# Kernel optimization log

Hardware: AMD Instinct MI355X
Metric: run time of the kernel (lower is better)

The kernel has to match this reference:

```python
import jax, jax.numpy as jnp
import numpy as np


def _dfb_filter():
    v = np.array([0.63, -0.193, 0.0972, -0.0526, 0.0272, -0.0144], dtype=np.float32)
    f = np.concatenate((v[::-1], v))
    f[::2] = -f[::2]
    return jnp.asarray(f)


def _resampm(x, type_, shift=1):
    # periodic shear along rows: out[..., i, j] = x[..., (i + k_j) % m, j]
    m, n = x.shape[-2], x.shape[-1]
    j = jnp.arange(n)
    k = (shift * j) % m if type_ == 1 else (-shift * j) % m
    rows = (jnp.arange(m)[:, None] + k[None, :]) % m  # [m, n]
    return x[..., rows, j[None, :]]


def _resamp(x, type_, shift=1):
    if type_ in (1, 2):
        return _resampm(x, type_, shift)
    return _resampm(x.swapaxes(-2, -1), type_ - 2, shift).swapaxes(-2, -1)


def _slice_1r(y):
    # interleave rows: [0, m, 1, m+1, ...]
    m = y.shape[-2] // 2
    a, b = y[..., :m, :], y[..., m:, :]
    return jnp.stack([a, b], axis=-2).reshape(y.shape)


def _slice_2c(y):
    # interleave cols: [0, n, 1, n+1, ...]
    n = y.shape[-1] // 2
    a, b = y[..., :n], y[..., n:]
    return jnp.stack([a, b], axis=-1).reshape(y.shape)


def _extend2(x, ru, rd, cl, cr, extmod):
    rx, cx = x.shape[-2], x.shape[-1]
    if extmod == 'per':
        y = jnp.concatenate([x[..., rx - ru:, :], x, x[..., :rd, :]], axis=-2)
    elif extmod == 'qper_col':
        cx2 = cx // 2  # cx is even here
        xs = jnp.concatenate([x[..., cx2:], x[..., :cx2]], axis=-1)
        y = jnp.concatenate([xs[..., rx - ru:, :], x, xs[..., :rd, :]], axis=-2)
    else:
        raise ValueError(extmod)
    return jnp.concatenate([y[..., cx - cl:], y, y[..., :cr]], axis=-1)


def _sep_conv(y, f):
    # depthwise separable filtering (torch used a dense diagonal kernel -> identical math)
    L = f.shape[0]
    ch = y.shape[1]
    dn = ('NCHW', 'OIHW', 'NCHW')
    kh = jnp.broadcast_to(f.reshape(1, 1, L, 1), (ch, 1, L, 1))
    y = jax.lax.conv_general_dilated(y, kh, (1, 1), 'VALID', dimension_numbers=dn, feature_group_count=ch)
    kw = jnp.broadcast_to(f.reshape(1, 1, 1, L), (ch, 1, 1, L))
    return jax.lax.conv_general_dilated(y, kw, (1, 1), 'VALID', dimension_numbers=dn, feature_group_count=ch)


def _sefilter2(x, f, extmod='per', shift=(0, 0)):
    L = f.shape[0]
    lf = (L - 1) / 2  # 5.5 for the 12-tap filter
    ru = int(np.floor(lf)) + shift[0]
    rd = int(np.ceil(lf)) - shift[0]
    cl = int(np.floor(lf)) + shift[1]
    cr = int(np.ceil(lf)) - shift[1]
    y = _extend2(x, ru, rd, cl, cr, extmod)
    return _sep_conv(y, f)


def _qprec(p0, p1, type2):
    if type2 == '1r':
        a = _resamp(p0, 4)
        b = jnp.roll(_resamp(p1, 4), 1, axis=-1)
        y = _slice_1r(jnp.concatenate([a, b], axis=-2))
        return _resamp(y, 1)
    elif type2 == '2c':
        a = _resamp(p0, 2)
        b = jnp.roll(_resamp(p1, 2), 1, axis=-2)
        y = _slice_2c(jnp.concatenate([a, b], axis=-1))
        return _resamp(y, 3)
    raise ValueError(type2)


def _fbrec(y0, y1, f, type2, extmod):
    p1 = -(2.0 ** -0.5) * (y1 + _sefilter2(y0, f, extmod))
    p0 = (2.0 ** 0.5) * y0 + _sefilter2(p1, f, extmod, (1, 1))
    return _qprec(p0, p1, type2)


def _dfbrec4(y0, y1, y2, y3):
    # dfbrec_layer for n=2 (4 directional subbands):
    # list reorder y[2:] = y[-1:1:-1] -> [y0, y1, y3, y2]; rebacksamp is a no-op for n=2.
    f = _dfb_filter()
    C = y0.shape[1]
    # new_fbrec_layer([y[1], y[3]], [y[0], y[2]], f, 'q', '2c', 'per')  (channel-batched)
    Y0 = jnp.concatenate([y1, y2], axis=1)
    Y1 = jnp.concatenate([y0, y3], axis=1)
    x = _fbrec(Y0, Y1, f, '2c', 'per')  # [N, 2C, H, 2W]
    x0, x1 = x[:, :C], x[:, C:]
    # fbrec_layer(x0, x1, f, 'q', '1r', 'qper_col')  -> [N, C, 2H, 2W]
    return _fbrec(x0, x1, f, '1r', 'qper_col')


def setup_inputs() -> dict:
    key = jax.random.key(0)
    ks = jax.random.split(key, 4)
    shp = (8, 32, 128, 128)
    return {('y%d' % i): jax.random.normal(ks[i], shp, dtype=jnp.float32) for i in range(4)}


def reference(y0, y1, y2, y3):
    return _dfbrec4(y0, y1, y2, y3)
```

## Files before the change

### kernel.cpp

```cpp
#include <hip/hip_runtime.h>

namespace {

constexpr float FF[12] = {0.0144f, 0.0272f, 0.0526f, 0.0972f, 0.193f, 0.63f,
                          -0.63f, -0.193f, -0.0972f, -0.0526f, -0.0272f, -0.0144f};
constexpr float SQ2   = 1.41421356237309515f;
constexpr float NISQ2 = -0.70710678118654752f;

template <int O, int W4>
__device__ __forceinline__ float4 hconv(const float4* R4, int row4, int j4) {
  float r[20];
#pragma unroll
  for (int d = 0; d < 5; ++d) {
    float4 t = R4[row4 + ((j4 + d - 2) & (W4 - 1))];
    r[4 * d + 0] = t.x; r[4 * d + 1] = t.y; r[4 * d + 2] = t.z; r[4 * d + 3] = t.w;
  }
  float4 o = make_float4(0.f, 0.f, 0.f, 0.f);
#pragma unroll
  for (int a = 0; a < 12; ++a) {
    const float fa = FF[a];
    o.x += fa * r[8 + 0 + a - O];
    o.y += fa * r[8 + 1 + a - O];
    o.z += fa * r[8 + 2 + a - O];
    o.w += fa * r[8 + 3 + a - O];
  }
  return o;
}

template <int O>
__device__ __forceinline__ float4 vconv_s1(const float4* S4, int i, int j4) {
  float4 o = make_float4(0.f, 0.f, 0.f, 0.f);
#pragma unroll
  for (int a = 0; a < 12; ++a) {
    const float fa = FF[a];
    float4 v = S4[((i + a - O) & 127) * 32 + j4];
    o.x += fa * v.x; o.y += fa * v.y; o.z += fa * v.z; o.w += fa * v.w;
  }
  return o;
}

template <int O>
__device__ __forceinline__ float4 vconv_s2(const float4* S4, int i, int j4) {
  float4 o = make_float4(0.f, 0.f, 0.f, 0.f);
#pragma unroll
  for (int a = 0; a < 12; ++a) {
    const float fa = FF[a];
    int r = i + a - O;
    int idx = ((unsigned)r < 128u) ? (r * 64 + j4) : ((r & 127) * 64 + (j4 ^ 32));
    float4 v = S4[idx];
    o.x += fa * v.x; o.y += fa * v.y; o.z += fa * v.z; o.w += fa * v.w;
  }
  return o;
}

}

__global__ __launch_bounds__(1024) void s1_kernel(
    const float* __restrict__ y0, const float* __restrict__ y1,
    const float* __restrict__ y2, const float* __restrict__ y3,
    float* __restrict__ xout) {
  __shared__ float bufA[16384];
  __shared__ float bufB[16384];
  float4* A4 = reinterpret_cast<float4*>(bufA);
  float4* B4 = reinterpret_cast<float4*>(bufB);

  const int p  = blockIdx.x;
  const int b  = p >> 6;
  const int cc = p & 63;
  const int sub = (b * 32 + (cc & 31)) << 14;
  const float* Y0 = (cc < 32 ? y1 : y2) + sub;
  const float* Y1 = (cc < 32 ? y0 : y3) + sub;
  const float4* Y04 = reinterpret_cast<const float4*>(Y0);
  const float4* Y14 = reinterpret_cast<const float4*>(Y1);
  float* xp = xout + (size_t)p * 32768;

  const int tid = threadIdx.x;

#pragma unroll
  for (int k = 0; k < 4; ++k) A4[tid + k * 1024] = Y04[tid + k * 1024];
  __syncthreads();

#pragma unroll
  for (int k = 0; k < 4; ++k) {
    int g = tid + k * 1024;
    B4[g] = vconv_s1<5>(A4, g >> 5, g & 31);
  }
  __syncthreads();

#pragma unroll
  for (int k = 0; k < 4; ++k) {
    int g = tid + k * 1024;
    int i = g >> 5, j4 = g & 31;
    float4 h = hconv<5, 32>(B4, i * 32, j4);
    float4 yv = Y14[g];
    float4 o;
    o.x = NISQ2 * (yv.x + h.x);
    o.y = NISQ2 * (yv.y + h.y);
    o.z = NISQ2 * (yv.z + h.z);
    o.w = NISQ2 * (yv.w + h.w);
    A4[g] = o;
  }
  __syncthreads();

#pragma unroll
  for (int k = 0; k < 4; ++k) {
    int g = tid + k * 1024;
    B4[g] = vconv_s1<6>(A4, g >> 5, g & 31);
  }
  __syncthreads();

  float4 pv[4];
#pragma unroll
  for (int k = 0; k < 4; ++k) {
    int g = tid + k * 1024;
    int i = g >> 5, j4 = g & 31;
    float4 h = hconv<6, 32>(B4, i * 32, j4);
    float4 yv = Y04[g];
    pv[k].x = SQ2 * yv.x + h.x;
    pv[k].y = SQ2 * yv.y + h.y;
    pv[k].z = SQ2 * yv.z + h.z;
    pv[k].w = SQ2 * yv.w + h.w;
  }
  __syncthreads();
#pragma unroll
  for (int k = 0; k < 4; ++k) B4[tid + k * 1024] = pv[k];
  __syncthreads();

#pragma unroll
  for (int k = 0; k < 8; ++k) {
    int t = tid + k * 1024;
    int i = t >> 6;
    int j4b = (t & 63) << 2;
    float tmp[4];
#pragma unroll
    for (int m = 0; m < 4; ++m) {
      int jo = j4b + m;
      int J = (i + jo) & 255;
      int c = J >> 1;
      float v;
      if (J & 1) {
        int r = (i - 1 - c) & 127;
        v = bufA[r * 128 + c];
      } else {
        int r = (i - c) & 127;
        v = bufB[r * 128 + c];
      }
      tmp[m] = v;
    }
    reinterpret_cast<float4*>(xp)[t] = make_float4(tmp[0], tmp[1], tmp[2], tmp[3]);
  }
}

__global__ __launch_bounds__(1024) void s2_kernel(const float* __restrict__ x,
                                                  float* __restrict__ out) {
  __shared__ float buf[32768];
  float4* X4 = reinterpret_cast<float4*>(buf);

  const int q = blockIdx.x;
  const int b = q >> 5, c = q & 31;
  const float* x0 = x + (size_t)(b * 64 + c) * 32768;
  const float* x1 = x + (size_t)(b * 64 + 32 + c) * 32768;
  const float4* x04 = reinterpret_cast<const float4*>(x0);
  const float4* x14 = reinterpret_cast<const float4*>(x1);
  float* op = out + (size_t)q * 65536;

  const int tid = threadIdx.x;
  float4 tv[8];

#pragma unroll
  for (int k = 0; k < 8; ++k) X4[tid + k * 1024] = x04[tid + k * 1024];
  __syncthreads();

#pragma unroll
  for (int k = 0; k < 8; ++k) {
    int g = tid + k * 1024;
    tv[k] = vconv_s2<5>(X4, g >> 6, g & 63);
  }
  __syncthreads();
#pragma unroll
  for (int k = 0; k < 8; ++k) X4[tid + k * 1024] = tv[k];
  __syncthreads();

#pragma unroll
  for (int k = 0; k < 8; ++k) {
    int g = tid + k * 1024;
    int i = g >> 6, j4 = g & 63;
    float4 h = hconv<5, 64>(X4, i * 64, j4);
    float4 xv = x14[g];
    tv[k].x = NISQ2 * (xv.x + h.x);
    tv[k].y = NISQ2 * (xv.y + h.y);
    tv[k].z = NISQ2 * (xv.z + h.z);
    tv[k].w = NISQ2 * (xv.w + h.w);
  }
  __syncthreads();
#pragma unroll
  for (int k = 0; k < 8; ++k) X4[tid + k * 1024] = tv[k];
  __syncthreads();

#pragma unroll
  for (int k = 0; k < 32; ++k) {
    int t = tid + k * 1024;
    int i = t >> 7;
    int u = t & 127;
    int jo = (u << 1) | ((i + 1) & 1);
    int r = ((i + jo) & 255) >> 1;
    int cc2 = (jo - 1 - r) & 255;
    op[i * 256 + jo] = buf[r * 256 + cc2];
  }

#pragma unroll
  for (int k = 0; k < 8; ++k) {
    int g = tid + k * 1024;
    tv[k] = vconv_s2<6>(X4, g >> 6, g & 63);
  }
  __syncthreads();
#pragma unroll
  for (int k = 0; k < 8; ++k) X4[tid + k * 1024] = tv[k];
  __syncthreads();

#pragma unroll
  for (int k = 0; k < 8; ++k) {
    int g = tid + k * 1024;
    int i = g >> 6, j4 = g & 63;
    float4 h = hconv<6, 64>(X4, i * 64, j4);
    float4 xv = x04[g];
    tv[k].x = SQ2 * xv.x + h.x;
    tv[k].y = SQ2 * xv.y + h.y;
    tv[k].z = SQ2 * xv.z + h.z;
    tv[k].w = SQ2 * xv.w + h.w;
  }
  __syncthreads();
#pragma unroll
  for (int k = 0; k < 8; ++k) X4[tid + k * 1024] = tv[k];
  __syncthreads();

#pragma unroll
  for (int k = 0; k < 32; ++k) {
    int t = tid + k * 1024;
    int i = t >> 7;
    int u = t & 127;
    int jo = (u << 1) | (i & 1);
    int r = ((i + jo) & 255) >> 1;
    int cc2 = (jo - r) & 255;
    op[i * 256 + jo] = buf[r * 256 + cc2];
  }
}

extern "C" void kernel_launch(void* const* d_in, const int* in_sizes, int n_in,
                              void* d_out, int out_size, void* d_ws, size_t ws_size,
                              hipStream_t stream) {
  const float* y0 = (const float*)d_in[0];
  const float* y1 = (const float*)d_in[1];
  const float* y2 = (const float*)d_in[2];
  const float* y3 = (const float*)d_in[3];
  float* xws = (float*)d_ws;
  float* outp = (float*)d_out;

  s1_kernel<<<512, 1024, 0, stream>>>(y0, y1, y2, y3, xws);
  s2_kernel<<<256, 1024, 0, stream>>>(xws, outp);
}
```

Baseline: 196.3 us.

## Register-block separable convolutions, pad shared rows, single buffer, vectorized output stores

Both kernels now compute the vertical filter with each thread producing 8 consecutive rows from a 19-row sliding window, and the horizontal filter with each thread producing 32 consecutive outputs from a 48-float register window. The aim is to cut redundant shared-memory reads. Shared rows are padded (stride 33/65 float4) to avoid bank conflicts, and s1 drops to one buffer with 512 threads. The odd-phase output values are gathered into registers before the buffer is overwritten, so the final write can emit interleaved float4 stores instead of scalar or split writes. The cost is higher register pressure (48-float windows plus 32 saved values), which may limit occupancy despite the launch-bounds hints.

```diff
diff --git a/kernel.cpp b/kernel.cpp
--- a/kernel.cpp
+++ b/kernel.cpp
@@ -7,62 +7,19 @@
 constexpr float SQ2   = 1.41421356237309515f;
 constexpr float NISQ2 = -0.70710678118654752f;
 
-template <int O, int W4>
-__device__ __forceinline__ float4 hconv(const float4* R4, int row4, int j4) {
-  float r[20];
-#pragma unroll
-  for (int d = 0; d < 5; ++d) {
-    float4 t = R4[row4 + ((j4 + d - 2) & (W4 - 1))];
-    r[4 * d + 0] = t.x; r[4 * d + 1] = t.y; r[4 * d + 2] = t.z; r[4 * d + 3] = t.w;
-  }
-  float4 o = make_float4(0.f, 0.f, 0.f, 0.f);
-#pragma unroll
-  for (int a = 0; a < 12; ++a) {
-    const float fa = FF[a];
-    o.x += fa * r[8 + 0 + a - O];
-    o.y += fa * r[8 + 1 + a - O];
-    o.z += fa * r[8 + 2 + a - O];
-    o.w += fa * r[8 + 3 + a - O];
-  }
-  return o;
-}
-
-template <int O>
-__device__ __forceinline__ float4 vconv_s1(const float4* S4, int i, int j4) {
-  float4 o = make_float4(0.f, 0.f, 0.f, 0.f);
-#pragma unroll
-  for (int a = 0; a < 12; ++a) {
-    const float fa = FF[a];
-    float4 v = S4[((i + a - O) & 127) * 32 + j4];
-    o.x += fa * v.x; o.y += fa * v.y; o.z += fa * v.z; o.w += fa * v.w;
-  }
-  return o;
-}
-
-template <int O>
-__device__ __forceinline__ float4 vconv_s2(const float4* S4, int i, int j4) {
-  float4 o = make_float4(0.f, 0.f, 0.f, 0.f);
-#pragma unroll
-  for (int a = 0; a < 12; ++a) {
-    const float fa = FF[a];
-    int r = i + a - O;
-    int idx = ((unsigned)r < 128u) ? (r * 64 + j4) : ((r & 127) * 64 + (j4 ^ 32));
-    float4 v = S4[idx];
-    o.x += fa * v.x; o.y += fa * v.y; o.z += fa * v.z; o.w += fa * v.w;
-  }
-  return o;
-}
-
-}
-
-__global__ __launch_bounds__(1024) void s1_kernel(
+__device__ __forceinline__ void fma4(float4& o, float s, const float4& v) {
+  o.x += s * v.x; o.y += s * v.y; o.z += s * v.z; o.w += s * v.w;
+}
+
+}
+
+__global__ __launch_bounds__(512, 4) void s1_kernel(
     const float* __restrict__ y0, const float* __restrict__ y1,
     const float* __restrict__ y2, const float* __restrict__ y3,
     float* __restrict__ xout) {
-  __shared__ float bufA[16384];
-  __shared__ float bufB[16384];
-  float4* A4 = reinterpret_cast<float4*>(bufA);
-  float4* B4 = reinterpret_cast<float4*>(bufB);
+  __shared__ float bufF[128 * 132];
+  float4* buf4 = reinterpret_cast<float4*>(bufF);
+  constexpr int SG = 33;
 
   const int p  = blockIdx.x;
   const int b  = p >> 6;
@@ -72,177 +29,341 @@
   const float* Y1 = (cc < 32 ? y0 : y3) + sub;
   const float4* Y04 = reinterpret_cast<const float4*>(Y0);
   const float4* Y14 = reinterpret_cast<const float4*>(Y1);
-  float* xp = xout + (size_t)p * 32768;
+  float4* xp4 = reinterpret_cast<float4*>(xout + (size_t)p * 32768);
 
   const int tid = threadIdx.x;
 
 #pragma unroll
-  for (int k = 0; k < 4; ++k) A4[tid + k * 1024] = Y04[tid + k * 1024];
-  __syncthreads();
-
-#pragma unroll
-  for (int k = 0; k < 4; ++k) {
-    int g = tid + k * 1024;
-    B4[g] = vconv_s1<5>(A4, g >> 5, g & 31);
-  }
-  __syncthreads();
-
-#pragma unroll
-  for (int k = 0; k < 4; ++k) {
-    int g = tid + k * 1024;
-    int i = g >> 5, j4 = g & 31;
-    float4 h = hconv<5, 32>(B4, i * 32, j4);
-    float4 yv = Y14[g];
-    float4 o;
-    o.x = NISQ2 * (yv.x + h.x);
-    o.y = NISQ2 * (yv.y + h.y);
-    o.z = NISQ2 * (yv.z + h.z);
-    o.w = NISQ2 * (yv.w + h.w);
-    A4[g] = o;
-  }
-  __syncthreads();
-
-#pragma unroll
-  for (int k = 0; k < 4; ++k) {
-    int g = tid + k * 1024;
-    B4[g] = vconv_s1<6>(A4, g >> 5, g & 31);
-  }
-  __syncthreads();
-
-  float4 pv[4];
-#pragma unroll
-  for (int k = 0; k < 4; ++k) {
-    int g = tid + k * 1024;
-    int i = g >> 5, j4 = g & 31;
-    float4 h = hconv<6, 32>(B4, i * 32, j4);
-    float4 yv = Y04[g];
-    pv[k].x = SQ2 * yv.x + h.x;
-    pv[k].y = SQ2 * yv.y + h.y;
-    pv[k].z = SQ2 * yv.z + h.z;
-    pv[k].w = SQ2 * yv.w + h.w;
-  }
-  __syncthreads();
-#pragma unroll
-  for (int k = 0; k < 4; ++k) B4[tid + k * 1024] = pv[k];
-  __syncthreads();
-
-#pragma unroll
   for (int k = 0; k < 8; ++k) {
-    int t = tid + k * 1024;
-    int i = t >> 6;
-    int j4b = (t & 63) << 2;
-    float tmp[4];
-#pragma unroll
-    for (int m = 0; m < 4; ++m) {
-      int jo = j4b + m;
-      int J = (i + jo) & 255;
+    int idx = tid + k * 512;
+    buf4[(idx >> 5) * SG + (idx & 31)] = Y04[idx];
+  }
+  __syncthreads();
+
+  {
+    const int j4 = tid & 31;
+    const int i0 = (tid >> 5) * 8;
+    float4 acc[8];
+#pragma unroll
+    for (int k = 0; k < 8; ++k) acc[k] = make_float4(0.f, 0.f, 0.f, 0.f);
+#pragma unroll
+    for (int d = 0; d < 19; ++d) {
+      int r = (i0 - 5 + d) & 127;
+      float4 v = buf4[r * SG + j4];
+#pragma unroll
+      for (int k = 0; k < 8; ++k) {
+        int a = d - k;
+        if (a >= 0 && a < 12) fma4(acc[k], FF[a], v);
+      }
+    }
+    __syncthreads();
+#pragma unroll
+    for (int k = 0; k < 8; ++k) buf4[(i0 + k) * SG + j4] = acc[k];
+  }
+  __syncthreads();
+
+  {
+    const int i  = tid >> 2;
+    const int g0 = (tid & 3) * 8;
+    float w[48];
+#pragma unroll
+    for (int d = 0; d < 12; ++d) {
+      float4 v = buf4[i * SG + ((g0 - 2 + d) & 31)];
+      w[4 * d + 0] = v.x; w[4 * d + 1] = v.y; w[4 * d + 2] = v.z; w[4 * d + 3] = v.w;
+    }
+    float4 pv[8];
+#pragma unroll
+    for (int mg = 0; mg < 8; ++mg) {
+      float4 yv = Y14[i * 32 + g0 + mg];
+      float o0 = 0.f, o1 = 0.f, o2 = 0.f, o3 = 0.f;
+#pragma unroll
+      for (int a = 0; a < 12; ++a) {
+        const float fa = FF[a];
+        o0 += fa * w[3 + 4 * mg + 0 + a];
+        o1 += fa * w[3 + 4 * mg + 1 + a];
+        o2 += fa * w[3 + 4 * mg + 2 + a];
+        o3 += fa * w[3 + 4 * mg + 3 + a];
+      }
+      pv[mg].x = NISQ2 * (yv.x + o0);
+      pv[mg].y = NISQ2 * (yv.y + o1);
+      pv[mg].z = NISQ2 * (yv.z + o2);
+      pv[mg].w = NISQ2 * (yv.w + o3);
+    }
+    __syncthreads();
+#pragma unroll
+    for (int mg = 0; mg < 8; ++mg) buf4[i * SG + g0 + mg] = pv[mg];
+  }
+  __syncthreads();
+
+  float xodd[32];
+  {
+#pragma unroll
+    for (int k = 0; k < 16; ++k) {
+      int t = tid + k * 512;
+      int i2 = t >> 6;
+      int j4o = t & 63;
+      int m0 = 1 - (i2 & 1);
+#pragma unroll
+      for (int h = 0; h < 2; ++h) {
+        int jo = 4 * j4o + m0 + 2 * h;
+        int J = (i2 + jo) & 255;
+        int c = J >> 1;
+        int r = (i2 - 1 - c) & 127;
+        xodd[2 * k + h] = bufF[r * 132 + c];
+      }
+    }
+    const int j4 = tid & 31;
+    const int i0 = (tid >> 5) * 8;
+    float4 acc[8];
+#pragma unroll
+    for (int k = 0; k < 8; ++k) acc[k] = make_float4(0.f, 0.f, 0.f, 0.f);
+#pragma unroll
+    for (int d = 0; d < 19; ++d) {
+      int r = (i0 - 6 + d) & 127;
+      float4 v = buf4[r * SG + j4];
+#pragma unroll
+      for (int k = 0; k < 8; ++k) {
+        int a = d - k;
+        if (a >= 0 && a < 12) fma4(acc[k], FF[a], v);
+      }
+    }
+    __syncthreads();
+#pragma unroll
+    for (int k = 0; k < 8; ++k) buf4[(i0 + k) * SG + j4] = acc[k];
+  }
+  __syncthreads();
+
+  {
+    const int i  = tid >> 2;
+    const int g0 = (tid & 3) * 8;
+    float w[48];
+#pragma unroll
+    for (int d = 0; d < 12; ++d) {
+      float4 v = buf4[i * SG + ((g0 - 2 + d) & 31)];
+      w[4 * d + 0] = v.x; w[4 * d + 1] = v.y; w[4 * d + 2] = v.z; w[4 * d + 3] = v.w;
+    }
+    float4 pv[8];
+#pragma unroll
+    for (int mg = 0; mg < 8; ++mg) {
+      float4 yv = Y04[i * 32 + g0 + mg];
+      float o0 = 0.f, o1 = 0.f, o2 = 0.f, o3 = 0.f;
+#pragma unroll
+      for (int a = 0; a < 12; ++a) {
+        const float fa = FF[a];
+        o0 += fa * w[2 + 4 * mg + 0 + a];
+        o1 += fa * w[2 + 4 * mg + 1 + a];
+        o2 += fa * w[2 + 4 * mg + 2 + a];
+        o3 += fa * w[2 + 4 * mg + 3 + a];
+      }
+      pv[mg].x = SQ2 * yv.x + o0;
+      pv[mg].y = SQ2 * yv.y + o1;
+      pv[mg].z = SQ2 * yv.z + o2;
+      pv[mg].w = SQ2 * yv.w + o3;
+    }
+    __syncthreads();
+#pragma unroll
+    for (int mg = 0; mg < 8; ++mg) buf4[i * SG + g0 + mg] = pv[mg];
+  }
+  __syncthreads();
+
+#pragma unroll
+  for (int k = 0; k < 16; ++k) {
+    int t = tid + k * 512;
+    int i2 = t >> 6;
+    int j4o = t & 63;
+    float ev[2];
+#pragma unroll
+    for (int h = 0; h < 2; ++h) {
+      int me = (i2 & 1) + 2 * h;
+      int jo = 4 * j4o + me;
+      int J = (i2 + jo) & 255;
       int c = J >> 1;
-      float v;
-      if (J & 1) {
-        int r = (i - 1 - c) & 127;
-        v = bufA[r * 128 + c];
-      } else {
-        int r = (i - c) & 127;
-        v = bufB[r * 128 + c];
-      }
-      tmp[m] = v;
-    }
-    reinterpret_cast<float4*>(xp)[t] = make_float4(tmp[0], tmp[1], tmp[2], tmp[3]);
-  }
-}
-
-__global__ __launch_bounds__(1024) void s2_kernel(const float* __restrict__ x,
-                                                  float* __restrict__ out) {
-  __shared__ float buf[32768];
-  float4* X4 = reinterpret_cast<float4*>(buf);
+      int r = (i2 - c) & 127;
+      ev[h] = bufF[r * 132 + c];
+    }
+    float o0 = xodd[2 * k + 0], o1 = xodd[2 * k + 1];
+    bool sw = (i2 & 1) != 0;
+    float t0 = sw ? o0 : ev[0];
+    float t1 = sw ? ev[0] : o0;
+    float t2 = sw ? o1 : ev[1];
+    float t3 = sw ? ev[1] : o1;
+    xp4[t] = make_float4(t0, t1, t2, t3);
+  }
+}
+
+__global__ __launch_bounds__(1024, 4) void s2_kernel(const float* __restrict__ x,
+                                                     float* __restrict__ out) {
+  __shared__ float bufF[128 * 260];
+  float4* buf4 = reinterpret_cast<float4*>(bufF);
+  constexpr int SG = 65;
 
   const int q = blockIdx.x;
   const int b = q >> 5, c = q & 31;
-  const float* x0 = x + (size_t)(b * 64 + c) * 32768;
-  const float* x1 = x + (size_t)(b * 64 + 32 + c) * 32768;
-  const float4* x04 = reinterpret_cast<const float4*>(x0);
-  const float4* x14 = reinterpret_cast<const float4*>(x1);
-  float* op = out + (size_t)q * 65536;
+  const float4* x04 = reinterpret_cast<const float4*>(x + (size_t)(b * 64 + c) * 32768);
+  const float4* x14 = reinterpret_cast<const float4*>(x + (size_t)(b * 64 + 32 + c) * 32768);
+  float4* op4 = reinterpret_cast<float4*>(out + (size_t)q * 65536);
 
   const int tid = threadIdx.x;
-  float4 tv[8];
-
-#pragma unroll
-  for (int k = 0; k < 8; ++k) X4[tid + k * 1024] = x04[tid + k * 1024];
-  __syncthreads();
 
 #pragma unroll
   for (int k = 0; k < 8; ++k) {
-    int g = tid + k * 1024;
-    tv[k] = vconv_s2<5>(X4, g >> 6, g & 63);
-  }
-  __syncthreads();
-#pragma unroll
-  for (int k = 0; k < 8; ++k) X4[tid + k * 1024] = tv[k];
-  __syncthreads();
-
-#pragma unroll
-  for (int k = 0; k < 8; ++k) {
-    int g = tid + k * 1024;
-    int i = g >> 6, j4 = g & 63;
-    float4 h = hconv<5, 64>(X4, i * 64, j4);
-    float4 xv = x14[g];
-    tv[k].x = NISQ2 * (xv.x + h.x);
-    tv[k].y = NISQ2 * (xv.y + h.y);
-    tv[k].z = NISQ2 * (xv.z + h.z);
-    tv[k].w = NISQ2 * (xv.w + h.w);
-  }
-  __syncthreads();
-#pragma unroll
-  for (int k = 0; k < 8; ++k) X4[tid + k * 1024] = tv[k];
-  __syncthreads();
-
-#pragma unroll
-  for (int k = 0; k < 32; ++k) {
+    int idx = tid + k * 1024;
+    buf4[(idx >> 6) * SG + (idx & 63)] = x04[idx];
+  }
+  __syncthreads();
+
+  {
+    const int j4 = tid & 63;
+    const int i0 = (tid >> 6) * 8;
+    float4 acc[8];
+#pragma unroll
+    for (int k = 0; k < 8; ++k) acc[k] = make_float4(0.f, 0.f, 0.f, 0.f);
+#pragma unroll
+    for (int d = 0; d < 19; ++d) {
+      int rr = i0 - 5 + d;
+      int r = rr & 127;
+      int g = ((unsigned)rr < 128u) ? j4 : (j4 ^ 32);
+      float4 v = buf4[r * SG + g];
+#pragma unroll
+      for (int k = 0; k < 8; ++k) {
+        int a = d - k;
+        if (a >= 0 && a < 12) fma4(acc[k], FF[a], v);
+      }
+    }
+    __syncthreads();
+#pragma unroll
+    for (int k = 0; k < 8; ++k) buf4[(i0 + k) * SG + j4] = acc[k];
+  }
+  __syncthreads();
+
+  {
+    const int i  = tid >> 3;
+    const int g0 = (tid & 7) * 8;
+    float w[48];
+#pragma unroll
+    for (int d = 0; d < 12; ++d) {
+      float4 v = buf4[i * SG + ((g0 - 2 + d) & 63)];
+      w[4 * d + 0] = v.x; w[4 * d + 1] = v.y; w[4 * d + 2] = v.z; w[4 * d + 3] = v.w;
+    }
+    float4 pv[8];
+#pragma unroll
+    for (int mg = 0; mg < 8; ++mg) {
+      float4 xv = x14[i * 64 + g0 + mg];
+      float o0 = 0.f, o1 = 0.f, o2 = 0.f, o3 = 0.f;
+#pragma unroll
+      for (int a = 0; a < 12; ++a) {
+        const float fa = FF[a];
+        o0 += fa * w[3 + 4 * mg + 0 + a];
+        o1 += fa * w[3 + 4 * mg + 1 + a];
+        o2 += fa * w[3 + 4 * mg + 2 + a];
+        o3 += fa * w[3 + 4 * mg + 3 + a];
+      }
+      pv[mg].x = NISQ2 * (xv.x + o0);
+      pv[mg].y = NISQ2 * (xv.y + o1);
+      pv[mg].z = NISQ2 * (xv.z + o2);
+      pv[mg].w = NISQ2 * (xv.w + o3);
+    }
+    __syncthreads();
+#pragma unroll
+    for (int mg = 0; mg < 8; ++mg) buf4[i * SG + g0 + mg] = pv[mg];
+  }
+  __syncthreads();
+
+  float oodd[32];
+  {
+#pragma unroll
+    for (int k = 0; k < 16; ++k) {
+      int t = tid + k * 1024;
+      int i2 = t >> 6;
+      int j4o = t & 63;
+      int m0 = 1 - (i2 & 1);
+#pragma unroll
+      for (int h = 0; h < 2; ++h) {
+        int jo = 4 * j4o + m0 + 2 * h;
+        int I = (i2 + jo) & 255;
+        int r2 = I >> 1;
+        int c2 = (jo - 1 - r2) & 255;
+        oodd[2 * k + h] = bufF[r2 * 260 + c2];
+      }
+    }
+    const int j4 = tid & 63;
+    const int i0 = (tid >> 6) * 8;
+    float4 acc[8];
+#pragma unroll
+    for (int k = 0; k < 8; ++k) acc[k] = make_float4(0.f, 0.f, 0.f, 0.f);
+#pragma unroll
+    for (int d = 0; d < 19; ++d) {
+      int rr = i0 - 6 + d;
+      int r = rr & 127;
+      int g = ((unsigned)rr < 128u) ? j4 : (j4 ^ 32);
+      float4 v = buf4[r * SG + g];
+#pragma unroll
+      for (int k = 0; k < 8; ++k) {
+        int a = d - k;
+        if (a >= 0 && a < 12) fma4(acc[k], FF[a], v);
+      }
+    }
+    __syncthreads();
+#pragma unroll
+    for (int k = 0; k < 8; ++k) buf4[(i0 + k) * SG + j4] = acc[k];
+  }
+  __syncthreads();
+
+  {
+    const int i  = tid >> 3;
+    const int g0 = (tid & 7) * 8;
+    float w[48];
+#pragma unroll
+    for (int d = 0; d < 12; ++d) {
+      float4 v = buf4[i * SG + ((g0 - 2 + d) & 63)];
+      w[4 * d + 0] = v.x; w[4 * d + 1] = v.y; w[4 * d + 2] = v.z; w[4 * d + 3] = v.w;
+    }
+    float4 pv[8];
+#pragma unroll
+    for (int mg = 0; mg < 8; ++mg) {
+      float4 xv = x04[i * 64 + g0 + mg];
+      float o0 = 0.f, o1 = 0.f, o2 = 0.f, o3 = 0.f;
+#pragma unroll
+      for (int a = 0; a < 12; ++a) {
+        const float fa = FF[a];
+        o0 += fa * w[2 + 4 * mg + 0 + a];
+        o1 += fa * w[2 + 4 * mg + 1 + a];
+        o2 += fa * w[2 + 4 * mg + 2 + a];
+        o3 += fa * w[2 + 4 * mg + 3 + a];
+      }
+      pv[mg].x = SQ2 * xv.x + o0;
+      pv[mg].y = SQ2 * xv.y + o1;
+      pv[mg].z = SQ2 * xv.z + o2;
+      pv[mg].w = SQ2 * xv.w + o3;
+    }
+    __syncthreads();
+#pragma unroll
+    for (int mg = 0; mg < 8; ++mg) buf4[i * SG + g0 + mg] = pv[mg];
+  }
+  __syncthreads();
+
+#pragma unroll
+  for (int k = 0; k < 16; ++k) {
     int t = tid + k * 1024;
-    int i = t >> 7;
-    int u = t & 127;
-    int jo = (u << 1) | ((i + 1) & 1);
-    int r = ((i + jo) & 255) >> 1;
-    int cc2 = (jo - 1 - r) & 255;
-    op[i * 256 + jo] = buf[r * 256 + cc2];
-  }
-
-#pragma unroll
-  for (int k = 0; k < 8; ++k) {
-    int g = tid + k * 1024;
-    tv[k] = vconv_s2<6>(X4, g >> 6, g & 63);
-  }
-  __syncthreads();
-#pragma unroll
-  for (int k = 0; k < 8; ++k) X4[tid + k * 1024] = tv[k];
-  __syncthreads();
-
-#pragma unroll
-  for (int k = 0; k < 8; ++k) {
-    int g = tid + k * 1024;
-    int i = g >> 6, j4 = g & 63;
-    float4 h = hconv<6, 64>(X4, i * 64, j4);
-    float4 xv = x04[g];
-    tv[k].x = SQ2 * xv.x + h.x;
-    tv[k].y = SQ2 * xv.y + h.y;
-    tv[k].z = SQ2 * xv.z + h.z;
-    tv[k].w = SQ2 * xv.w + h.w;
-  }
-  __syncthreads();
-#pragma unroll
-  for (int k = 0; k < 8; ++k) X4[tid + k * 1024] = tv[k];
-  __syncthreads();
-
-#pragma unroll
-  for (int k = 0; k < 32; ++k) {
-    int t = tid + k * 1024;
-    int i = t >> 7;
-    int u = t & 127;
-    int jo = (u << 1) | (i & 1);
-    int r = ((i + jo) & 255) >> 1;
-    int cc2 = (jo - r) & 255;
-    op[i * 256 + jo] = buf[r * 256 + cc2];
+    int i2 = t >> 6;
+    int j4o = t & 63;
+    float ev[2];
+#pragma unroll
+    for (int h = 0; h < 2; ++h) {
+      int me = (i2 & 1) + 2 * h;
+      int jo = 4 * j4o + me;
+      int I = (i2 + jo) & 255;
+      int r2 = I >> 1;
+      int c2 = (jo - r2) & 255;
+      ev[h] = bufF[r2 * 260 + c2];
+    }
+    float o0 = oodd[2 * k + 0], o1 = oodd[2 * k + 1];
+    bool sw = (i2 & 1) != 0;
+    float t0 = sw ? o0 : ev[0];
+    float t1 = sw ? ev[0] : o0;
+    float t2 = sw ? o1 : ev[1];
+    float t3 = sw ? ev[1] : o1;
+    op4[t] = make_float4(t0, t1, t2, t3);
   }
 }
 
@@ -256,6 +377,6 @@
   float* xws = (float*)d_ws;
   float* outp = (float*)d_out;
 
-  s1_kernel<<<512, 1024, 0, stream>>>(y0, y1, y2, y3, xws);
+  s1_kernel<<<512, 512, 0, stream>>>(y0, y1, y2, y3, xws);
   s2_kernel<<<256, 1024, 0, stream>>>(xws, outp);
 }
```

Measured after the change: 201.4 us. +2.6%, slower.

## Fuse separable convolutions into register-blocked row sweeps with padded single LDS buffer

Applied to the files above, without the earlier changes.

Restructures both kernels so each thread computes an 8-row strip. It applies the horizontal filter per input row and accumulates the vertical filter in registers across a 19-row sliding window. This removes the intermediate LDS round trips and barriers between the vertical and horizontal passes, and the first pass now reads straight from global memory. A single padded LDS buffer replaces the two buffers to cut bank conflicts, and output stores become float4 writes that interleave odd and even phases held in registers. The price is some redundant horizontal work per strip, higher register pressure from the accumulators and saved odd values, and a smaller s1 block size.

```diff
diff --git a/kernel.cpp b/kernel.cpp
--- a/kernel.cpp
+++ b/kernel.cpp
@@ -7,242 +7,261 @@
 constexpr float SQ2   = 1.41421356237309515f;
 constexpr float NISQ2 = -0.70710678118654752f;
 
-template <int O, int W4>
-__device__ __forceinline__ float4 hconv(const float4* R4, int row4, int j4) {
-  float r[20];
-#pragma unroll
-  for (int d = 0; d < 5; ++d) {
-    float4 t = R4[row4 + ((j4 + d - 2) & (W4 - 1))];
-    r[4 * d + 0] = t.x; r[4 * d + 1] = t.y; r[4 * d + 2] = t.z; r[4 * d + 3] = t.w;
-  }
+__device__ __forceinline__ void fma4(float4& o, float s, const float4& v) {
+  o.x += s * v.x; o.y += s * v.y; o.z += s * v.z; o.w += s * v.w;
+}
+
+template <int SH>
+__device__ __forceinline__ float4 hrow_conv(const float* w) {
   float4 o = make_float4(0.f, 0.f, 0.f, 0.f);
 #pragma unroll
   for (int a = 0; a < 12; ++a) {
     const float fa = FF[a];
-    o.x += fa * r[8 + 0 + a - O];
-    o.y += fa * r[8 + 1 + a - O];
-    o.z += fa * r[8 + 2 + a - O];
-    o.w += fa * r[8 + 3 + a - O];
+    o.x += fa * w[SH + 0 + a];
+    o.y += fa * w[SH + 1 + a];
+    o.z += fa * w[SH + 2 + a];
+    o.w += fa * w[SH + 3 + a];
   }
   return o;
 }
 
-template <int O>
-__device__ __forceinline__ float4 vconv_s1(const float4* S4, int i, int j4) {
-  float4 o = make_float4(0.f, 0.f, 0.f, 0.f);
-#pragma unroll
-  for (int a = 0; a < 12; ++a) {
-    const float fa = FF[a];
-    float4 v = S4[((i + a - O) & 127) * 32 + j4];
-    o.x += fa * v.x; o.y += fa * v.y; o.z += fa * v.z; o.w += fa * v.w;
-  }
-  return o;
-}
-
-template <int O>
-__device__ __forceinline__ float4 vconv_s2(const float4* S4, int i, int j4) {
-  float4 o = make_float4(0.f, 0.f, 0.f, 0.f);
-#pragma unroll
-  for (int a = 0; a < 12; ++a) {
-    const float fa = FF[a];
-    int r = i + a - O;
-    int idx = ((unsigned)r < 128u) ? (r * 64 + j4) : ((r & 127) * 64 + (j4 ^ 32));
-    float4 v = S4[idx];
-    o.x += fa * v.x; o.y += fa * v.y; o.z += fa * v.z; o.w += fa * v.w;
-  }
-  return o;
-}
-
-}
-
-__global__ __launch_bounds__(1024) void s1_kernel(
+}
+
+__global__ __launch_bounds__(512, 4) void s1_kernel(
     const float* __restrict__ y0, const float* __restrict__ y1,
     const float* __restrict__ y2, const float* __restrict__ y3,
     float* __restrict__ xout) {
-  __shared__ float bufA[16384];
-  __shared__ float bufB[16384];
-  float4* A4 = reinterpret_cast<float4*>(bufA);
-  float4* B4 = reinterpret_cast<float4*>(bufB);
+  __shared__ float bufF[128 * 132];
+  float4* buf4 = reinterpret_cast<float4*>(bufF);
+  constexpr int SG = 33;
 
   const int p  = blockIdx.x;
   const int b  = p >> 6;
   const int cc = p & 63;
   const int sub = (b * 32 + (cc & 31)) << 14;
-  const float* Y0 = (cc < 32 ? y1 : y2) + sub;
-  const float* Y1 = (cc < 32 ? y0 : y3) + sub;
-  const float4* Y04 = reinterpret_cast<const float4*>(Y0);
-  const float4* Y14 = reinterpret_cast<const float4*>(Y1);
-  float* xp = xout + (size_t)p * 32768;
+  const float4* Y04 = reinterpret_cast<const float4*>((cc < 32 ? y1 : y2) + sub);
+  const float4* Y14 = reinterpret_cast<const float4*>((cc < 32 ? y0 : y3) + sub);
+  float4* xp4 = reinterpret_cast<float4*>(xout + (size_t)p * 32768);
 
   const int tid = threadIdx.x;
-
-#pragma unroll
-  for (int k = 0; k < 4; ++k) A4[tid + k * 1024] = Y04[tid + k * 1024];
-  __syncthreads();
-
-#pragma unroll
-  for (int k = 0; k < 4; ++k) {
-    int g = tid + k * 1024;
-    B4[g] = vconv_s1<5>(A4, g >> 5, g & 31);
-  }
-  __syncthreads();
-
-#pragma unroll
-  for (int k = 0; k < 4; ++k) {
-    int g = tid + k * 1024;
-    int i = g >> 5, j4 = g & 31;
-    float4 h = hconv<5, 32>(B4, i * 32, j4);
-    float4 yv = Y14[g];
-    float4 o;
-    o.x = NISQ2 * (yv.x + h.x);
-    o.y = NISQ2 * (yv.y + h.y);
-    o.z = NISQ2 * (yv.z + h.z);
-    o.w = NISQ2 * (yv.w + h.w);
-    A4[g] = o;
-  }
-  __syncthreads();
-
-#pragma unroll
-  for (int k = 0; k < 4; ++k) {
-    int g = tid + k * 1024;
-    B4[g] = vconv_s1<6>(A4, g >> 5, g & 31);
-  }
-  __syncthreads();
-
-  float4 pv[4];
-#pragma unroll
-  for (int k = 0; k < 4; ++k) {
-    int g = tid + k * 1024;
-    int i = g >> 5, j4 = g & 31;
-    float4 h = hconv<6, 32>(B4, i * 32, j4);
-    float4 yv = Y04[g];
-    pv[k].x = SQ2 * yv.x + h.x;
-    pv[k].y = SQ2 * yv.y + h.y;
-    pv[k].z = SQ2 * yv.z + h.z;
-    pv[k].w = SQ2 * yv.w + h.w;
-  }
-  __syncthreads();
-#pragma unroll
-  for (int k = 0; k < 4; ++k) B4[tid + k * 1024] = pv[k];
-  __syncthreads();
-
-#pragma unroll
-  for (int k = 0; k < 8; ++k) {
-    int t = tid + k * 1024;
-    int i = t >> 6;
-    int j4b = (t & 63) << 2;
-    float tmp[4];
-#pragma unroll
-    for (int m = 0; m < 4; ++m) {
-      int jo = j4b + m;
-      int J = (i + jo) & 255;
-      int c = J >> 1;
-      float v;
-      if (J & 1) {
-        int r = (i - 1 - c) & 127;
-        v = bufA[r * 128 + c];
-      } else {
-        int r = (i - c) & 127;
-        v = bufB[r * 128 + c];
-      }
-      tmp[m] = v;
-    }
-    reinterpret_cast<float4*>(xp)[t] = make_float4(tmp[0], tmp[1], tmp[2], tmp[3]);
-  }
-}
-
-__global__ __launch_bounds__(1024) void s2_kernel(const float* __restrict__ x,
-                                                  float* __restrict__ out) {
-  __shared__ float buf[32768];
-  float4* X4 = reinterpret_cast<float4*>(buf);
+  const int j  = tid & 31;
+  const int i0 = (tid >> 5) * 8;
+
+  float4 acc[8];
+#pragma unroll
+  for (int k = 0; k < 8; ++k) acc[k] = make_float4(0.f, 0.f, 0.f, 0.f);
+#pragma unroll
+  for (int d = 0; d < 19; ++d) {
+    const int r = (i0 + d - 5) & 127;
+    float w[20];
+#pragma unroll
+    for (int dg = 0; dg < 5; ++dg) {
+      float4 v = Y04[r * 32 + ((j + dg - 2) & 31)];
+      w[4 * dg + 0] = v.x; w[4 * dg + 1] = v.y; w[4 * dg + 2] = v.z; w[4 * dg + 3] = v.w;
+    }
+    const float4 h = hrow_conv<3>(w);
+#pragma unroll
+    for (int k = 0; k < 8; ++k) {
+      const int a = d - k;
+      if (a >= 0 && a < 12) fma4(acc[k], FF[a], h);
+    }
+  }
+#pragma unroll
+  for (int k = 0; k < 8; ++k) {
+    float4 yv = Y14[(i0 + k) * 32 + j];
+    float4 pv;
+    pv.x = NISQ2 * (yv.x + acc[k].x);
+    pv.y = NISQ2 * (yv.y + acc[k].y);
+    pv.z = NISQ2 * (yv.z + acc[k].z);
+    pv.w = NISQ2 * (yv.w + acc[k].w);
+    buf4[(i0 + k) * SG + j] = pv;
+  }
+  __syncthreads();
+
+  float xodd[32];
+#pragma unroll
+  for (int k = 0; k < 16; ++k) {
+    const int t = tid + k * 512;
+    const int i2 = t >> 6, j4o = t & 63;
+    const int m0 = 1 - (i2 & 1);
+#pragma unroll
+    for (int h = 0; h < 2; ++h) {
+      const int jo = 4 * j4o + m0 + 2 * h;
+      const int J = (i2 + jo) & 255;
+      const int c = J >> 1;
+      const int r = (i2 - 1 - c) & 127;
+      xodd[2 * k + h] = bufF[r * 132 + c];
+    }
+  }
+#pragma unroll
+  for (int k = 0; k < 8; ++k) acc[k] = make_float4(0.f, 0.f, 0.f, 0.f);
+#pragma unroll
+  for (int d = 0; d < 19; ++d) {
+    const int r = (i0 + d - 6) & 127;
+    float w[20];
+#pragma unroll
+    for (int dg = 0; dg < 5; ++dg) {
+      float4 v = buf4[r * SG + ((j + dg - 2) & 31)];
+      w[4 * dg + 0] = v.x; w[4 * dg + 1] = v.y; w[4 * dg + 2] = v.z; w[4 * dg + 3] = v.w;
+    }
+    const float4 h = hrow_conv<2>(w);
+#pragma unroll
+    for (int k = 0; k < 8; ++k) {
+      const int a = d - k;
+      if (a >= 0 && a < 12) fma4(acc[k], FF[a], h);
+    }
+  }
+  float4 pv[8];
+#pragma unroll
+  for (int k = 0; k < 8; ++k) {
+    float4 yv = Y04[(i0 + k) * 32 + j];
+    pv[k].x = SQ2 * yv.x + acc[k].x;
+    pv[k].y = SQ2 * yv.y + acc[k].y;
+    pv[k].z = SQ2 * yv.z + acc[k].z;
+    pv[k].w = SQ2 * yv.w + acc[k].w;
+  }
+  __syncthreads();
+#pragma unroll
+  for (int k = 0; k < 8; ++k) buf4[(i0 + k) * SG + j] = pv[k];
+  __syncthreads();
+
+#pragma unroll
+  for (int k = 0; k < 16; ++k) {
+    const int t = tid + k * 512;
+    const int i2 = t >> 6, j4o = t & 63;
+    float ev[2];
+#pragma unroll
+    for (int h = 0; h < 2; ++h) {
+      const int me = (i2 & 1) + 2 * h;
+      const int jo = 4 * j4o + me;
+      const int J = (i2 + jo) & 255;
+      const int c = J >> 1;
+      const int r = (i2 - c) & 127;
+      ev[h] = bufF[r * 132 + c];
+    }
+    const float o0 = xodd[2 * k + 0], o1 = xodd[2 * k + 1];
+    const bool sw = (i2 & 1) != 0;
+    xp4[t] = make_float4(sw ? o0 : ev[0], sw ? ev[0] : o0,
+                         sw ? o1 : ev[1], sw ? ev[1] : o1);
+  }
+}
+
+__global__ __launch_bounds__(1024, 4) void s2_kernel(const float* __restrict__ x,
+                                                     float* __restrict__ out) {
+  __shared__ float bufF[128 * 260];
+  float4* buf4 = reinterpret_cast<float4*>(bufF);
+  constexpr int SG = 65;
 
   const int q = blockIdx.x;
   const int b = q >> 5, c = q & 31;
-  const float* x0 = x + (size_t)(b * 64 + c) * 32768;
-  const float* x1 = x + (size_t)(b * 64 + 32 + c) * 32768;
-  const float4* x04 = reinterpret_cast<const float4*>(x0);
-  const float4* x14 = reinterpret_cast<const float4*>(x1);
-  float* op = out + (size_t)q * 65536;
+  const float4* x04 = reinterpret_cast<const float4*>(x + (size_t)(b * 64 + c) * 32768);
+  const float4* x14 = reinterpret_cast<const float4*>(x + (size_t)(b * 64 + 32 + c) * 32768);
+  float4* op4 = reinterpret_cast<float4*>(out + (size_t)q * 65536);
 
   const int tid = threadIdx.x;
-  float4 tv[8];
-
-#pragma unroll
-  for (int k = 0; k < 8; ++k) X4[tid + k * 1024] = x04[tid + k * 1024];
-  __syncthreads();
-
-#pragma unroll
-  for (int k = 0; k < 8; ++k) {
-    int g = tid + k * 1024;
-    tv[k] = vconv_s2<5>(X4, g >> 6, g & 63);
-  }
-  __syncthreads();
-#pragma unroll
-  for (int k = 0; k < 8; ++k) X4[tid + k * 1024] = tv[k];
-  __syncthreads();
-
-#pragma unroll
-  for (int k = 0; k < 8; ++k) {
-    int g = tid + k * 1024;
-    int i = g >> 6, j4 = g & 63;
-    float4 h = hconv<5, 64>(X4, i * 64, j4);
-    float4 xv = x14[g];
-    tv[k].x = NISQ2 * (xv.x + h.x);
-    tv[k].y = NISQ2 * (xv.y + h.y);
-    tv[k].z = NISQ2 * (xv.z + h.z);
-    tv[k].w = NISQ2 * (xv.w + h.w);
-  }
-  __syncthreads();
-#pragma unroll
-  for (int k = 0; k < 8; ++k) X4[tid + k * 1024] = tv[k];
-  __syncthreads();
-
-#pragma unroll
-  for (int k = 0; k < 32; ++k) {
-    int t = tid + k * 1024;
-    int i = t >> 7;
-    int u = t & 127;
-    int jo = (u << 1) | ((i + 1) & 1);
-    int r = ((i + jo) & 255) >> 1;
-    int cc2 = (jo - 1 - r) & 255;
-    op[i * 256 + jo] = buf[r * 256 + cc2];
-  }
-
-#pragma unroll
-  for (int k = 0; k < 8; ++k) {
-    int g = tid + k * 1024;
-    tv[k] = vconv_s2<6>(X4, g >> 6, g & 63);
-  }
-  __syncthreads();
-#pragma unroll
-  for (int k = 0; k < 8; ++k) X4[tid + k * 1024] = tv[k];
-  __syncthreads();
-
-#pragma unroll
-  for (int k = 0; k < 8; ++k) {
-    int g = tid + k * 1024;
-    int i = g >> 6, j4 = g & 63;
-    float4 h = hconv<6, 64>(X4, i * 64, j4);
-    float4 xv = x04[g];
-    tv[k].x = SQ2 * xv.x + h.x;
-    tv[k].y = SQ2 * xv.y + h.y;
-    tv[k].z = SQ2 * xv.z + h.z;
-    tv[k].w = SQ2 * xv.w + h.w;
-  }
-  __syncthreads();
-#pragma unroll
-  for (int k = 0; k < 8; ++k) X4[tid + k * 1024] = tv[k];
-  __syncthreads();
-
-#pragma unroll
-  for (int k = 0; k < 32; ++k) {
-    int t = tid + k * 1024;
-    int i = t >> 7;
-    int u = t & 127;
-    int jo = (u << 1) | (i & 1);
-    int r = ((i + jo) & 255) >> 1;
-    int cc2 = (jo - r) & 255;
-    op[i * 256 + jo] = buf[r * 256 + cc2];
+  const int j  = tid & 63;
+  const int i0 = (tid >> 6) * 8;
+
+  float4 acc[8];
+#pragma unroll
+  for (int k = 0; k < 8; ++k) acc[k] = make_float4(0.f, 0.f, 0.f, 0.f);
+#pragma unroll
+  for (int d = 0; d < 19; ++d) {
+    const int rr = i0 + d - 5;
+    const int r = rr & 127;
+    const int gx = ((unsigned)rr < 128u) ? 0 : 32;
+    float w[20];
+#pragma unroll
+    for (int dg = 0; dg < 5; ++dg) {
+      float4 v = x04[r * 64 + (((j + dg - 2) & 63) ^ gx)];
+      w[4 * dg + 0] = v.x; w[4 * dg + 1] = v.y; w[4 * dg + 2] = v.z; w[4 * dg + 3] = v.w;
+    }
+    const float4 h = hrow_conv<3>(w);
+#pragma unroll
+    for (int k = 0; k < 8; ++k) {
+      const int a = d - k;
+      if (a >= 0 && a < 12) fma4(acc[k], FF[a], h);
+    }
+  }
+#pragma unroll
+  for (int k = 0; k < 8; ++k) {
+    float4 xv = x14[(i0 + k) * 64 + j];
+    float4 pv;
+    pv.x = NISQ2 * (xv.x + acc[k].x);
+    pv.y = NISQ2 * (xv.y + acc[k].y);
+    pv.z = NISQ2 * (xv.z + acc[k].z);
+    pv.w = NISQ2 * (xv.w + acc[k].w);
+    buf4[(i0 + k) * SG + j] = pv;
+  }
+  __syncthreads();
+
+  float oodd[32];
+#pragma unroll
+  for (int k = 0; k < 16; ++k) {
+    const int t = tid + k * 1024;
+    const int i2 = t >> 6, j4o = t & 63;
+    const int m0 = 1 - (i2 & 1);
+#pragma unroll
+    for (int h = 0; h < 2; ++h) {
+      const int jo = 4 * j4o + m0 + 2 * h;
+      const int I = (i2 + jo) & 255;
+      const int r2 = I >> 1;
+      const int c2 = (jo - 1 - r2) & 255;
+      oodd[2 * k + h] = bufF[r2 * 260 + c2];
+    }
+  }
+#pragma unroll
+  for (int k = 0; k < 8; ++k) acc[k] = make_float4(0.f, 0.f, 0.f, 0.f);
+#pragma unroll
+  for (int d = 0; d < 19; ++d) {
+    const int rr = i0 + d - 6;
+    const int r = rr & 127;
+    const int gx = ((unsigned)rr < 128u) ? 0 : 32;
+    float w[20];
+#pragma unroll
+    for (int dg = 0; dg < 5; ++dg) {
+      float4 v = buf4[r * SG + (((j + dg - 2) & 63) ^ gx)];
+      w[4 * dg + 0] = v.x; w[4 * dg + 1] = v.y; w[4 * dg + 2] = v.z; w[4 * dg + 3] = v.w;
+    }
+    const float4 h = hrow_conv<2>(w);
+#pragma unroll
+    for (int k = 0; k < 8; ++k) {
+      const int a = d - k;
+      if (a >= 0 && a < 12) fma4(acc[k], FF[a], h);
+    }
+  }
+  float4 pv[8];
+#pragma unroll
+  for (int k = 0; k < 8; ++k) {
+    float4 xv = x04[(i0 + k) * 64 + j];
+    pv[k].x = SQ2 * xv.x + acc[k].x;
+    pv[k].y = SQ2 * xv.y + acc[k].y;
+    pv[k].z = SQ2 * xv.z + acc[k].z;
+    pv[k].w = SQ2 * xv.w + acc[k].w;
+  }
+  __syncthreads();
+#pragma unroll
+  for (int k = 0; k < 8; ++k) buf4[(i0 + k) * SG + j] = pv[k];
+  __syncthreads();
+
+#pragma unroll
+  for (int k = 0; k < 16; ++k) {
+    const int t = tid + k * 1024;
+    const int i2 = t >> 6, j4o = t & 63;
+    float ev[2];
+#pragma unroll
+    for (int h = 0; h < 2; ++h) {
+      const int me = (i2 & 1) + 2 * h;
+      const int jo = 4 * j4o + me;
+      const int I = (i2 + jo) & 255;
+      const int r2 = I >> 1;
+      const int c2 = (jo - r2) & 255;
+      ev[h] = bufF[r2 * 260 + c2];
+    }
+    const float o0 = oodd[2 * k + 0], o1 = oodd[2 * k + 1];
+    const bool sw = (i2 & 1) != 0;
+    op4[t] = make_float4(sw ? o0 : ev[0], sw ? ev[0] : o0,
+                         sw ? o1 : ev[1], sw ? ev[1] : o1);
   }
 }
 
@@ -256,6 +275,6 @@
   float* xws = (float*)d_ws;
   float* outp = (float*)d_out;
 
-  s1_kernel<<<512, 1024, 0, stream>>>(y0, y1, y2, y3, xws);
+  s1_kernel<<<512, 512, 0, stream>>>(y0, y1, y2, y3, xws);
   s2_kernel<<<256, 1024, 0, stream>>>(xws, outp);
 }
```

After: 242.7 us. 23.6% more time.
